# Kernel tuning notes

Hardware: AMD Instinct MI355X
Metric: run time of the kernel (lower is better)

Reference implementation:

```python
import jax, jax.numpy as jnp
import numpy as np

N = 50000      # nodes
E = 800000     # edges (before self loops)
F_DIM = 512    # raw feature dim
HID = 64       # hidden dim (= per-head dim, concat=False)
HEADS = 4
EMB = 64
NEG_SLOPE = 0.2
LN_EPS = 1e-5


def setup_inputs() -> dict:
    key = jax.random.key(0)
    ks = jax.random.split(key, 24)
    rn = lambda k, shape: jax.random.normal(k, shape, dtype=jnp.float32) * 0.05
    inp = {
        'features': jax.random.normal(ks[0], (N, F_DIM), dtype=jnp.float32),
        'edge_index': jax.random.randint(ks[1], (2, E), 0, N),
        'Wt': rn(ks[2], (F_DIM, HID)), 'bt': jnp.zeros((HID,), jnp.float32),
        'Wp': rn(ks[3], (HID, EMB)), 'bp': jnp.zeros((EMB,), jnp.float32),
    }
    for l in range(2):
        o = 4 + l * 4
        inp[f'Wg{l}'] = rn(ks[o], (HID, HEADS * HID))
        inp[f'as{l}'] = rn(ks[o + 1], (HEADS, HID))
        inp[f'ad{l}'] = rn(ks[o + 2], (HEADS, HID))
        inp[f'bg{l}'] = jnp.zeros((HID,), jnp.float32)
        inp[f'g{l}'] = jnp.ones((HID,), jnp.float32)
        inp[f'b{l}'] = jnp.zeros((HID,), jnp.float32)
        inp[f'a{l}'] = jnp.full((1,), 0.25, jnp.float32)  # PReLU weight
    return inp


def gat_block(x, src, dst, Wg, a_src, a_dst, bg, gamma, beta, prelu_a):
    # GATConv (heads=HEADS, concat=False, add_self_loops already in src/dst)
    h = (x @ Wg).reshape(N, HEADS, HID)                    # [N,H,C]
    al_s = jnp.einsum('nhc,hc->nh', h, a_src)              # [N,H]
    al_d = jnp.einsum('nhc,hc->nh', h, a_dst)
    e = jax.nn.leaky_relu(al_s[src] + al_d[dst], NEG_SLOPE)  # [E,H]
    m = jax.ops.segment_max(e, dst, num_segments=N)
    ex = jnp.exp(e - m[dst])
    denom = jax.ops.segment_sum(ex, dst, num_segments=N)
    alpha = ex / denom[dst]                                # segment softmax over in-edges
    out = jax.ops.segment_sum(h[src] * alpha[:, :, None], dst, num_segments=N)  # [N,H,C]
    out = out.mean(axis=1) + bg                            # concat=False -> mean heads
    # LayerNorm
    mu = out.mean(-1, keepdims=True)
    var = ((out - mu) ** 2).mean(-1, keepdims=True)
    xn = (out - mu) / jnp.sqrt(var + LN_EPS) * gamma + beta
    # PReLU
    return jnp.where(xn > 0, xn, prelu_a * xn)


def reference(features, edge_index, Wt, bt, Wp, bp,
              Wg0, as0, ad0, bg0, g0, b0, a0,
              Wg1, as1, ad1, bg1, g1, b1, a1):
    loops = jnp.arange(N)
    src = jnp.concatenate([edge_index[0], loops])
    dst = jnp.concatenate([edge_index[1], loops])
    x = features @ Wt + bt
    x = x + gat_block(x, src, dst, Wg0, as0, ad0, bg0, g0, b0, a0)
    x = x + gat_block(x, src, dst, Wg1, as1, ad1, bg1, g1, b1, a1)
    z = x @ Wp + bp
    return z / jnp.maximum(jnp.linalg.norm(z, axis=-1, keepdims=True), 1e-12)
```

## Files before the change

kernel.cpp:

```cpp
#include <hip/hip_runtime.h>
#include <hip/hip_bf16.h>

typedef __attribute__((ext_vector_type(8))) short bvec8;
typedef __attribute__((ext_vector_type(4))) float fvec4;

__device__ __forceinline__ void splitf(float f, short& hi, short& lo) {
  __hip_bfloat16 h = __float2bfloat16(f);
  float r = f - __bfloat162float(h);
  __hip_bfloat16 l = __float2bfloat16(r);
  hi = *(short*)&h;
  lo = *(short*)&l;
}
__device__ __forceinline__ float bits2f(unsigned short u) {
  unsigned int v = ((unsigned int)u) << 16;
  return __uint_as_float(v);
}

__global__ void k_degree(const int* __restrict__ ei, int* __restrict__ cnt, int E, int N) {
  int i = blockIdx.x * 256 + threadIdx.x;
  if (i >= E + N) return;
  int d = (i < E) ? ei[E + i] : (i - E);
  atomicAdd(&cnt[d], 1);
}

__global__ void k_scan(const int* __restrict__ cnt, int* __restrict__ off, int* __restrict__ cur, int N) {
  __shared__ int wsum[16];
  __shared__ int s_carry;
  int t = threadIdx.x, lane = t & 63, wv = t >> 6;
  if (t == 0) s_carry = 0;
  __syncthreads();
  for (int base = 0; base < N; base += 4096) {
    int idx = base + t * 4;
    int4 v = make_int4(0, 0, 0, 0);
    if (idx < N) v = *(const int4*)(cnt + idx);
    int s0 = v.x, s1 = s0 + v.y, s2 = s1 + v.z, s3 = s2 + v.w;
    int sc = s3;
    #pragma unroll
    for (int d = 1; d < 64; d <<= 1) {
      int u = __shfl_up(sc, d, 64);
      if (lane >= d) sc += u;
    }
    if (lane == 63) wsum[wv] = sc;
    __syncthreads();
    int carry = s_carry;
    int woff = 0;
    #pragma unroll
    for (int w = 0; w < 16; ++w) woff += (w < wv) ? wsum[w] : 0;
    int eb = carry + woff + sc - s3;
    if (idx < N) {
      int4 o = make_int4(eb, eb + s0, eb + s1, eb + s2);
      *(int4*)(off + idx) = o;
      *(int4*)(cur + idx) = o;
    }
    __syncthreads();
    if (t == 1023) s_carry = carry + woff + sc;
    __syncthreads();
  }
  if (t == 0) off[N] = s_carry;
}

__global__ void k_scatter(const int* __restrict__ ei, int* __restrict__ cur, int* __restrict__ csr, int E, int N) {
  int i = blockIdx.x * 256 + threadIdx.x;
  if (i >= E + N) return;
  int s, d;
  if (i < E) { s = ei[i]; d = ei[E + i]; } else { s = i - E; d = i - E; }
  int p = atomicAdd(&cur[d], 1);
  csr[p] = s;
}

__global__ __launch_bounds__(64) void k_wprep(const float* __restrict__ Wg, short* __restrict__ pk) {
  int tile = blockIdx.x;
  int lane = threadIdx.x;
  int w = tile >> 3, s = (tile >> 2) & 1, ct = tile & 3;
  int fq = lane >> 4, fr = lane & 15;
  bvec8 hv, lv;
  #pragma unroll
  for (int j = 0; j < 8; ++j) {
    short hh, ll;
    splitf(Wg[(size_t)(s * 32 + fq * 8 + j) * 256 + w * 64 + ct * 16 + fr], hh, ll);
    hv[j] = hh; lv[j] = ll;
  }
  *(bvec8*)(pk + tile * 1024 + lane * 8) = hv;
  *(bvec8*)(pk + tile * 1024 + 512 + lane * 8) = lv;
}

#define LROW 56
__global__ __launch_bounds__(256) void k_x0(const float* __restrict__ feat, const float* __restrict__ Wt,
                                            const float* __restrict__ bt, float* __restrict__ x, int N) {
  __shared__ __align__(16) short sAh[64 * LROW];
  __shared__ __align__(16) short sAl[64 * LROW];
  __shared__ __align__(16) short sBh[64 * LROW];
  __shared__ __align__(16) short sBl[64 * LROW];

  const int t = threadIdx.x;
  const int lane = t & 63;
  const int w = t >> 6;
  const int fr = lane & 15;
  const int fq = lane >> 4;
  const int n0 = blockIdx.x * 64;

  const int ar = t >> 2;
  const int ac8 = (t & 3) * 8;
  int arow = n0 + ar; if (arow >= N) arow = N - 1;
  const float* fbase = feat + (size_t)arow * 512;
  const int bn = t & 63;
  const int bc8 = (t >> 6) * 8;

  fvec4 acc[4];
  #pragma unroll
  for (int i = 0; i < 4; ++i) acc[i] = (fvec4){0.f, 0.f, 0.f, 0.f};

  for (int s = 0; s < 16; ++s) {
    const int k0 = s * 32;
    __syncthreads();
    {
      float4 f0 = *(const float4*)(fbase + k0 + ac8);
      float4 f1 = *(const float4*)(fbase + k0 + ac8 + 4);
      float fv[8] = {f0.x, f0.y, f0.z, f0.w, f1.x, f1.y, f1.z, f1.w};
      bvec8 hv, lv;
      #pragma unroll
      for (int j = 0; j < 8; ++j) { short h, l; splitf(fv[j], h, l); hv[j] = h; lv[j] = l; }
      *(bvec8*)(sAh + ar * LROW + ac8) = hv;
      *(bvec8*)(sAl + ar * LROW + ac8) = lv;
    }
    {
      bvec8 hv, lv;
      #pragma unroll
      for (int j = 0; j < 8; ++j) {
        float v = Wt[(size_t)(k0 + bc8 + j) * 64 + bn];
        short h, l; splitf(v, h, l); hv[j] = h; lv[j] = l;
      }
      *(bvec8*)(sBh + bn * LROW + bc8) = hv;
      *(bvec8*)(sBl + bn * LROW + bc8) = lv;
    }
    __syncthreads();
    const bvec8 ah = *(const bvec8*)(sAh + (w * 16 + fr) * LROW + fq * 8);
    const bvec8 al = *(const bvec8*)(sAl + (w * 16 + fr) * LROW + fq * 8);
    #pragma unroll
    for (int nt = 0; nt < 4; ++nt) {
      const bvec8 bh = *(const bvec8*)(sBh + (nt * 16 + fr) * LROW + fq * 8);
      const bvec8 bl = *(const bvec8*)(sBl + (nt * 16 + fr) * LROW + fq * 8);
      acc[nt] = __builtin_amdgcn_mfma_f32_16x16x32_bf16(ah, bh, acc[nt], 0, 0, 0);
      acc[nt] = __builtin_amdgcn_mfma_f32_16x16x32_bf16(ah, bl, acc[nt], 0, 0, 0);
      acc[nt] = __builtin_amdgcn_mfma_f32_16x16x32_bf16(al, bh, acc[nt], 0, 0, 0);
    }
  }
  #pragma unroll
  for (int nt = 0; nt < 4; ++nt) {
    float btv = bt[nt * 16 + fr];
    #pragma unroll
    for (int r = 0; r < 4; ++r) {
      int node = n0 + w * 16 + fq * 4 + r;
      if (node < N) x[(size_t)node * 64 + nt * 16 + fr] = acc[nt][r] + btv;
    }
  }
}

#define HROW 72
__global__ __launch_bounds__(256) void k_h(const float* __restrict__ x, const short* __restrict__ pk,
                                           const float* __restrict__ as_, const float* __restrict__ ad_,
                                           __hip_bfloat16* __restrict__ h, float* __restrict__ als,
                                           float* __restrict__ ald, int N) {
  __shared__ __align__(16) short sAh[64 * HROW];
  __shared__ __align__(16) short sAl[64 * HROW];
  const int t = threadIdx.x;
  const int lane = t & 63;
  const int w = t >> 6;
  const int fr = lane & 15;
  const int fq = lane >> 4;
  const int n0 = blockIdx.x * 64;

  {
    int ar = t >> 2;
    int c0 = (t & 3) * 16;
    int arow = n0 + ar; if (arow >= N) arow = N - 1;
    const float* xb = x + (size_t)arow * 64 + c0;
    #pragma unroll
    for (int half = 0; half < 2; ++half) {
      float4 f0 = *(const float4*)(xb + half * 8);
      float4 f1 = *(const float4*)(xb + half * 8 + 4);
      float fv[8] = {f0.x, f0.y, f0.z, f0.w, f1.x, f1.y, f1.z, f1.w};
      bvec8 hv, lv;
      #pragma unroll
      for (int j = 0; j < 8; ++j) { short hh, ll; splitf(fv[j], hh, ll); hv[j] = hh; lv[j] = ll; }
      *(bvec8*)(sAh + ar * HROW + c0 + half * 8) = hv;
      *(bvec8*)(sAl + ar * HROW + c0 + half * 8) = lv;
    }
  }
  bvec8 bh[2][4], bl[2][4];
  #pragma unroll
  for (int s = 0; s < 2; ++s)
    #pragma unroll
    for (int ct = 0; ct < 4; ++ct) {
      int tile = (w * 2 + s) * 4 + ct;
      bh[s][ct] = *(const bvec8*)(pk + tile * 1024 + lane * 8);
      bl[s][ct] = *(const bvec8*)(pk + tile * 1024 + 512 + lane * 8);
    }
  __syncthreads();
  fvec4 acc[4][4];
  #pragma unroll
  for (int nt = 0; nt < 4; ++nt)
    #pragma unroll
    for (int ct = 0; ct < 4; ++ct) acc[nt][ct] = (fvec4){0.f, 0.f, 0.f, 0.f};
  #pragma unroll
  for (int s = 0; s < 2; ++s)
    #pragma unroll
    for (int nt = 0; nt < 4; ++nt) {
      const bvec8 ah = *(const bvec8*)(sAh + (nt * 16 + fr) * HROW + s * 32 + fq * 8);
      const bvec8 al = *(const bvec8*)(sAl + (nt * 16 + fr) * HROW + s * 32 + fq * 8);
      #pragma unroll
      for (int ct = 0; ct < 4; ++ct) {
        acc[nt][ct] = __builtin_amdgcn_mfma_f32_16x16x32_bf16(ah, bh[s][ct], acc[nt][ct], 0, 0, 0);
        acc[nt][ct] = __builtin_amdgcn_mfma_f32_16x16x32_bf16(ah, bl[s][ct], acc[nt][ct], 0, 0, 0);
        acc[nt][ct] = __builtin_amdgcn_mfma_f32_16x16x32_bf16(al, bh[s][ct], acc[nt][ct], 0, 0, 0);
      }
    }
  float asv[4], adv[4];
  #pragma unroll
  for (int ct = 0; ct < 4; ++ct) {
    asv[ct] = as_[w * 64 + ct * 16 + fr];
    adv[ct] = ad_[w * 64 + ct * 16 + fr];
  }
  #pragma unroll
  for (int nt = 0; nt < 4; ++nt) {
    #pragma unroll
    for (int r = 0; r < 4; ++r) {
      int n = n0 + nt * 16 + fq * 4 + r;
      float ps = 0.f, pd = 0.f;
      #pragma unroll
      for (int ct = 0; ct < 4; ++ct) {
        ps = fmaf(acc[nt][ct][r], asv[ct], ps);
        pd = fmaf(acc[nt][ct][r], adv[ct], pd);
      }
      #pragma unroll
      for (int m = 1; m < 16; m <<= 1) { ps += __shfl_xor(ps, m, 64); pd += __shfl_xor(pd, m, 64); }
      if (fr == 0 && n < N) { als[(size_t)n * 4 + w] = ps; ald[(size_t)n * 4 + w] = pd; }
      #pragma unroll
      for (int ct = 0; ct < 4; ++ct)
        if (n < N) h[(size_t)n * 256 + w * 64 + ct * 16 + fr] = __float2bfloat16(acc[nt][ct][r]);
    }
  }
}

template <bool FINAL>
__global__ __launch_bounds__(256) void k_agg(const __hip_bfloat16* __restrict__ h, const float* __restrict__ als,
                                             const float* __restrict__ ald, const int* __restrict__ off,
                                             const int* __restrict__ csr, const float* __restrict__ bg,
                                             const float* __restrict__ gam, const float* __restrict__ bet,
                                             const float* __restrict__ pa, float* __restrict__ x,
                                             const float* __restrict__ Wp, const float* __restrict__ bp,
                                             float* __restrict__ out, int N) {
  int lane = threadIdx.x & 63;
  int n = blockIdx.x * 4 + (threadIdx.x >> 6);
  if (n >= N) return;
  int hh = lane >> 4;
  int cg = (lane & 15) * 4;
  float aldv = ald[(size_t)n * 4 + hh];
  int e0 = __builtin_amdgcn_readfirstlane(off[n]);
  int e1 = __builtin_amdgcn_readfirstlane(off[n + 1]);
  float a0 = 0, a1 = 0, a2 = 0, a3 = 0, den = 0;
  const unsigned short* hb = (const unsigned short*)h;
  const int co = hh * 64 + cg;
  int e = e0;
  for (; e + 4 <= e1; e += 4) {
    int s0 = csr[e + 0], s1 = csr[e + 1], s2 = csr[e + 2], s3 = csr[e + 3];
    float q0 = als[(size_t)s0 * 4 + hh];
    float q1 = als[(size_t)s1 * 4 + hh];
    float q2 = als[(size_t)s2 * 4 + hh];
    float q3 = als[(size_t)s3 * 4 + hh];
    ushort4 g0 = *(const ushort4*)(hb + (size_t)s0 * 256 + co);
    ushort4 g1 = *(const ushort4*)(hb + (size_t)s1 * 256 + co);
    ushort4 g2 = *(const ushort4*)(hb + (size_t)s2 * 256 + co);
    ushort4 g3 = *(const ushort4*)(hb + (size_t)s3 * 256 + co);
    float t0 = q0 + aldv; t0 = fmaxf(t0, 0.2f * t0); float w0 = __expf(t0);
    float t1 = q1 + aldv; t1 = fmaxf(t1, 0.2f * t1); float w1 = __expf(t1);
    float t2 = q2 + aldv; t2 = fmaxf(t2, 0.2f * t2); float w2 = __expf(t2);
    float t3 = q3 + aldv; t3 = fmaxf(t3, 0.2f * t3); float w3 = __expf(t3);
    den += (w0 + w1) + (w2 + w3);
    a0 += w0 * bits2f(g0.x) + w1 * bits2f(g1.x) + w2 * bits2f(g2.x) + w3 * bits2f(g3.x);
    a1 += w0 * bits2f(g0.y) + w1 * bits2f(g1.y) + w2 * bits2f(g2.y) + w3 * bits2f(g3.y);
    a2 += w0 * bits2f(g0.z) + w1 * bits2f(g1.z) + w2 * bits2f(g2.z) + w3 * bits2f(g3.z);
    a3 += w0 * bits2f(g0.w) + w1 * bits2f(g1.w) + w2 * bits2f(g2.w) + w3 * bits2f(g3.w);
  }
  for (; e < e1; ++e) {
    int s = csr[e];
    float t = als[(size_t)s * 4 + hh] + aldv;
    t = fmaxf(t, 0.2f * t);
    float w = __expf(t);
    den += w;
    const ushort4 hv = *(const ushort4*)(hb + (size_t)s * 256 + co);
    a0 += w * bits2f(hv.x); a1 += w * bits2f(hv.y); a2 += w * bits2f(hv.z); a3 += w * bits2f(hv.w);
  }
  float inv = 1.0f / den;
  a0 *= inv; a1 *= inv; a2 *= inv; a3 *= inv;
  a0 += __shfl_xor(a0, 16, 64); a0 += __shfl_xor(a0, 32, 64);
  a1 += __shfl_xor(a1, 16, 64); a1 += __shfl_xor(a1, 32, 64);
  a2 += __shfl_xor(a2, 16, 64); a2 += __shfl_xor(a2, 32, 64);
  a3 += __shfl_xor(a3, 16, 64); a3 += __shfl_xor(a3, 32, 64);
  float v0 = a0 * 0.25f + bg[cg + 0];
  float v1 = a1 * 0.25f + bg[cg + 1];
  float v2 = a2 * 0.25f + bg[cg + 2];
  float v3 = a3 * 0.25f + bg[cg + 3];
  float sum = v0 + v1 + v2 + v3;
  #pragma unroll
  for (int m = 1; m < 16; m <<= 1) sum += __shfl_xor(sum, m, 64);
  float mu = sum * (1.f / 64.f);
  float d0 = v0 - mu, d1 = v1 - mu, d2 = v2 - mu, d3 = v3 - mu;
  float vv = d0 * d0 + d1 * d1 + d2 * d2 + d3 * d3;
  #pragma unroll
  for (int m = 1; m < 16; m <<= 1) vv += __shfl_xor(vv, m, 64);
  float rstd = rsqrtf(vv * (1.f / 64.f) + 1e-5f);
  float A = pa[0];
  float y0 = d0 * rstd * gam[cg + 0] + bet[cg + 0];
  float y1 = d1 * rstd * gam[cg + 1] + bet[cg + 1];
  float y2 = d2 * rstd * gam[cg + 2] + bet[cg + 2];
  float y3 = d3 * rstd * gam[cg + 3] + bet[cg + 3];
  y0 = y0 > 0.f ? y0 : A * y0;
  y1 = y1 > 0.f ? y1 : A * y1;
  y2 = y2 > 0.f ? y2 : A * y2;
  y3 = y3 > 0.f ? y3 : A * y3;
  float o0 = 0.f, o1 = 0.f, o2 = 0.f, o3 = 0.f;
  if (lane < 16) {
    float4 xo = *(const float4*)(x + (size_t)n * 64 + cg);
    o0 = xo.x + y0; o1 = xo.y + y1; o2 = xo.z + y2; o3 = xo.w + y3;
  }
  if (!FINAL) {
    if (lane < 16) {
      float4 o = make_float4(o0, o1, o2, o3);
      *(float4*)(x + (size_t)n * 64 + cg) = o;
    }
  } else {
    float acc = bp[lane];
    #pragma unroll
    for (int g = 0; g < 16; ++g) {
      float rx = __shfl(o0, g, 64), ry = __shfl(o1, g, 64);
      float rz = __shfl(o2, g, 64), rw = __shfl(o3, g, 64);
      const float* wp = Wp + g * 4 * 64 + lane;
      acc = fmaf(rx, wp[0],   acc);
      acc = fmaf(ry, wp[64],  acc);
      acc = fmaf(rz, wp[128], acc);
      acc = fmaf(rw, wp[192], acc);
    }
    float sq = acc * acc;
    #pragma unroll
    for (int m = 1; m < 64; m <<= 1) sq += __shfl_xor(sq, m, 64);
    float nrm = fmaxf(sqrtf(sq), 1e-12f);
    out[(size_t)n * 64 + lane] = acc / nrm;
  }
}

extern "C" void kernel_launch(void* const* d_in, const int* in_sizes, int n_in,
                              void* d_out, int out_size, void* d_ws, size_t ws_size,
                              hipStream_t stream) {
  const float* feat = (const float*)d_in[0];
  const int*   ei   = (const int*)d_in[1];
  const float* Wt   = (const float*)d_in[2];
  const float* bt   = (const float*)d_in[3];
  const float* Wp   = (const float*)d_in[4];
  const float* bp   = (const float*)d_in[5];
  const float* Wg[2]  = {(const float*)d_in[6],  (const float*)d_in[13]};
  const float* as_[2] = {(const float*)d_in[7],  (const float*)d_in[14]};
  const float* ad_[2] = {(const float*)d_in[8],  (const float*)d_in[15]};
  const float* bg[2]  = {(const float*)d_in[9],  (const float*)d_in[16]};
  const float* gm[2]  = {(const float*)d_in[10], (const float*)d_in[17]};
  const float* be[2]  = {(const float*)d_in[11], (const float*)d_in[18]};
  const float* pa[2]  = {(const float*)d_in[12], (const float*)d_in[19]};

  const int N = in_sizes[0] / 512;
  const int E = in_sizes[1] / 2;

  float* x = (float*)d_ws;
  __hip_bfloat16* hb = (__hip_bfloat16*)(x + (size_t)N * 64);
  float* als = (float*)((short*)hb + (size_t)N * 256);
  float* ald = als + (size_t)N * 4;
  int* cnt = (int*)(ald + (size_t)N * 4);
  int* cur = cnt + N;
  int* csr = cur + N;
  int* off = csr + (E + N);
  short* pk0 = (short*)(((uintptr_t)(off + N + 1) + 15) & ~(uintptr_t)15);
  short* pk1 = pk0 + 32768;

  hipMemsetAsync(cnt, 0, (size_t)N * sizeof(int), stream);
  int eb = (E + N + 255) / 256;
  k_degree<<<eb, 256, 0, stream>>>(ei, cnt, E, N);
  k_scan<<<1, 1024, 0, stream>>>(cnt, off, cur, N);
  k_scatter<<<eb, 256, 0, stream>>>(ei, cur, csr, E, N);
  k_wprep<<<32, 64, 0, stream>>>(Wg[0], pk0);
  k_wprep<<<32, 64, 0, stream>>>(Wg[1], pk1);

  int nb4 = (N + 3) / 4;
  int nb64 = (N + 63) / 64;
  k_x0<<<nb64, 256, 0, stream>>>(feat, Wt, bt, x, N);

  k_h<<<nb64, 256, 0, stream>>>(x, pk0, as_[0], ad_[0], hb, als, ald, N);
  k_agg<false><<<nb4, 256, 0, stream>>>(hb, als, ald, off, csr, bg[0], gm[0], be[0], pa[0], x,
                                        Wp, bp, (float*)d_out, N);
  k_h<<<nb64, 256, 0, stream>>>(x, pk1, as_[1], ad_[1], hb, als, ald, N);
  k_agg<true><<<nb4, 256, 0, stream>>>(hb, als, ald, off, csr, bg[1], gm[1], be[1], pa[1], x,
                                       Wp, bp, (float*)d_out, N);
}
```

Measured before the change: 489.0 us.

## Store x as pre-split bf16 hi/lo, prepack Wt, parallelize CSR scan

The node state x is now kept as two bf16 planes (hi and lo), so k_h feeds MFMA operands straight from global memory without an LDS staging pass and a per-use split. Wt is prepacked into MFMA fragment layout in a merged prep kernel, and k_x0 now handles 128 rows per block with no shared memory or barriers. The single-block sequential scan is replaced by a three-kernel block scan, top-level scan and add. This trades extra kernel launches and a slightly different rounding of x (hi+lo, roughly 16 mantissa bits) for fewer syncs and less LDS traffic.

Result: no change. 485.6 us (-0.7%).

```diff
diff --git a/kernel.cpp b/kernel.cpp
--- a/kernel.cpp
+++ b/kernel.cpp
@@ -23,40 +23,51 @@
   atomicAdd(&cnt[d], 1);
 }
 
-__global__ void k_scan(const int* __restrict__ cnt, int* __restrict__ off, int* __restrict__ cur, int N) {
+__global__ __launch_bounds__(1024) void k_scan_blk(const int* __restrict__ cnt, int* __restrict__ off,
+                                                   int* __restrict__ bsum, int N) {
   __shared__ int wsum[16];
-  __shared__ int s_carry;
   int t = threadIdx.x, lane = t & 63, wv = t >> 6;
-  if (t == 0) s_carry = 0;
+  int idx = blockIdx.x * 4096 + t * 4;
+  int4 v = make_int4(0, 0, 0, 0);
+  if (idx < N) v = *(const int4*)(cnt + idx);
+  int s0 = v.x, s1 = s0 + v.y, s2 = s1 + v.z, s3 = s2 + v.w;
+  int sc = s3;
+  #pragma unroll
+  for (int d = 1; d < 64; d <<= 1) {
+    int u = __shfl_up(sc, d, 64);
+    if (lane >= d) sc += u;
+  }
+  if (lane == 63) wsum[wv] = sc;
   __syncthreads();
-  for (int base = 0; base < N; base += 4096) {
-    int idx = base + t * 4;
-    int4 v = make_int4(0, 0, 0, 0);
-    if (idx < N) v = *(const int4*)(cnt + idx);
-    int s0 = v.x, s1 = s0 + v.y, s2 = s1 + v.z, s3 = s2 + v.w;
-    int sc = s3;
-    #pragma unroll
-    for (int d = 1; d < 64; d <<= 1) {
-      int u = __shfl_up(sc, d, 64);
-      if (lane >= d) sc += u;
-    }
-    if (lane == 63) wsum[wv] = sc;
-    __syncthreads();
-    int carry = s_carry;
-    int woff = 0;
-    #pragma unroll
-    for (int w = 0; w < 16; ++w) woff += (w < wv) ? wsum[w] : 0;
-    int eb = carry + woff + sc - s3;
-    if (idx < N) {
-      int4 o = make_int4(eb, eb + s0, eb + s1, eb + s2);
-      *(int4*)(off + idx) = o;
-      *(int4*)(cur + idx) = o;
-    }
-    __syncthreads();
-    if (t == 1023) s_carry = carry + woff + sc;
-    __syncthreads();
-  }
-  if (t == 0) off[N] = s_carry;
+  int woff = 0;
+  #pragma unroll
+  for (int w = 0; w < 16; ++w) woff += (w < wv) ? wsum[w] : 0;
+  int eb = woff + sc - s3;
+  if (idx < N) {
+    int4 o = make_int4(eb, eb + s0, eb + s1, eb + s2);
+    *(int4*)(off + idx) = o;
+  }
+  if (t == 1023) bsum[blockIdx.x] = woff + sc;
+}
+
+__global__ void k_scan_top(int* __restrict__ bsum, int* __restrict__ off, int nb, int N) {
+  if (threadIdx.x == 0) {
+    int ex = 0;
+    for (int i = 0; i < nb; ++i) { int tv = bsum[i]; bsum[i] = ex; ex += tv; }
+    off[N] = ex;
+  }
+}
+
+__global__ __launch_bounds__(1024) void k_scan_add(int* __restrict__ off, int* __restrict__ cur,
+                                                   const int* __restrict__ bsum, int N) {
+  int t = threadIdx.x;
+  int idx = blockIdx.x * 4096 + t * 4;
+  if (idx >= N) return;
+  int b = bsum[blockIdx.x];
+  int4 o = *(const int4*)(off + idx);
+  o.x += b; o.y += b; o.z += b; o.w += b;
+  *(int4*)(off + idx) = o;
+  *(int4*)(cur + idx) = o;
 }
 
 __global__ void k_scatter(const int* __restrict__ ei, int* __restrict__ cur, int* __restrict__ csr, int E, int N) {
@@ -68,30 +79,109 @@
   csr[p] = s;
 }
 
-__global__ __launch_bounds__(64) void k_wprep(const float* __restrict__ Wg, short* __restrict__ pk) {
-  int tile = blockIdx.x;
+__global__ __launch_bounds__(64) void k_prep(const float* __restrict__ Wg0, const float* __restrict__ Wg1,
+                                             const float* __restrict__ Wt,
+                                             short* __restrict__ pk0, short* __restrict__ pk1,
+                                             short* __restrict__ wtpk) {
+  int b = blockIdx.x;
   int lane = threadIdx.x;
-  int w = tile >> 3, s = (tile >> 2) & 1, ct = tile & 3;
   int fq = lane >> 4, fr = lane & 15;
   bvec8 hv, lv;
-  #pragma unroll
-  for (int j = 0; j < 8; ++j) {
-    short hh, ll;
-    splitf(Wg[(size_t)(s * 32 + fq * 8 + j) * 256 + w * 64 + ct * 16 + fr], hh, ll);
-    hv[j] = hh; lv[j] = ll;
-  }
-  *(bvec8*)(pk + tile * 1024 + lane * 8) = hv;
-  *(bvec8*)(pk + tile * 1024 + 512 + lane * 8) = lv;
-}
-
-#define LROW 56
-__global__ __launch_bounds__(256) void k_x0(const float* __restrict__ feat, const float* __restrict__ Wt,
-                                            const float* __restrict__ bt, float* __restrict__ x, int N) {
-  __shared__ __align__(16) short sAh[64 * LROW];
-  __shared__ __align__(16) short sAl[64 * LROW];
-  __shared__ __align__(16) short sBh[64 * LROW];
-  __shared__ __align__(16) short sBl[64 * LROW];
-
+  if (b < 64) {
+    const float* Wg = (b < 32) ? Wg0 : Wg1;
+    short* pk = (b < 32) ? pk0 : pk1;
+    int tile = b & 31;
+    int w = tile >> 3, s = (tile >> 2) & 1, ct = tile & 3;
+    #pragma unroll
+    for (int j = 0; j < 8; ++j) {
+      short hh, ll;
+      splitf(Wg[(size_t)(s * 32 + fq * 8 + j) * 256 + w * 64 + ct * 16 + fr], hh, ll);
+      hv[j] = hh; lv[j] = ll;
+    }
+    *(bvec8*)(pk + tile * 1024 + lane * 8) = hv;
+    *(bvec8*)(pk + tile * 1024 + 512 + lane * 8) = lv;
+  } else {
+    int tile = b - 64;
+    int s = tile >> 2, nt = tile & 3;
+    #pragma unroll
+    for (int j = 0; j < 8; ++j) {
+      short hh, ll;
+      splitf(Wt[(size_t)(s * 32 + fq * 8 + j) * 64 + nt * 16 + fr], hh, ll);
+      hv[j] = hh; lv[j] = ll;
+    }
+    *(bvec8*)(wtpk + tile * 1024 + lane * 8) = hv;
+    *(bvec8*)(wtpk + tile * 1024 + 512 + lane * 8) = lv;
+  }
+}
+
+__global__ __launch_bounds__(256) void k_x0(const float* __restrict__ feat, const short* __restrict__ wtpk,
+                                            const float* __restrict__ bt,
+                                            short* __restrict__ xhi, short* __restrict__ xlo, int N) {
+  const int t = threadIdx.x;
+  const int lane = t & 63;
+  const int w = t >> 6;
+  const int fr = lane & 15;
+  const int fq = lane >> 4;
+  const int n0 = blockIdx.x * 128;
+
+  int ar0 = n0 + w * 32 + fr;      if (ar0 >= N) ar0 = N - 1;
+  int ar1 = n0 + w * 32 + 16 + fr; if (ar1 >= N) ar1 = N - 1;
+  const float* fb0 = feat + (size_t)ar0 * 512 + fq * 8;
+  const float* fb1 = feat + (size_t)ar1 * 512 + fq * 8;
+
+  fvec4 acc[2][4];
+  #pragma unroll
+  for (int m = 0; m < 2; ++m)
+    #pragma unroll
+    for (int nt = 0; nt < 4; ++nt) acc[m][nt] = (fvec4){0.f, 0.f, 0.f, 0.f};
+
+  for (int s = 0; s < 16; ++s) {
+    bvec8 bh[4], bl[4];
+    #pragma unroll
+    for (int nt = 0; nt < 4; ++nt) {
+      bh[nt] = *(const bvec8*)(wtpk + (s * 4 + nt) * 1024 + lane * 8);
+      bl[nt] = *(const bvec8*)(wtpk + (s * 4 + nt) * 1024 + 512 + lane * 8);
+    }
+    #pragma unroll
+    for (int m = 0; m < 2; ++m) {
+      const float* fb = m ? fb1 : fb0;
+      float4 f0 = *(const float4*)(fb + s * 32);
+      float4 f1 = *(const float4*)(fb + s * 32 + 4);
+      float fv[8] = {f0.x, f0.y, f0.z, f0.w, f1.x, f1.y, f1.z, f1.w};
+      bvec8 ah, al;
+      #pragma unroll
+      for (int j = 0; j < 8; ++j) { short hh, ll; splitf(fv[j], hh, ll); ah[j] = hh; al[j] = ll; }
+      #pragma unroll
+      for (int nt = 0; nt < 4; ++nt) {
+        acc[m][nt] = __builtin_amdgcn_mfma_f32_16x16x32_bf16(ah, bh[nt], acc[m][nt], 0, 0, 0);
+        acc[m][nt] = __builtin_amdgcn_mfma_f32_16x16x32_bf16(ah, bl[nt], acc[m][nt], 0, 0, 0);
+        acc[m][nt] = __builtin_amdgcn_mfma_f32_16x16x32_bf16(al, bh[nt], acc[m][nt], 0, 0, 0);
+      }
+    }
+  }
+  #pragma unroll
+  for (int m = 0; m < 2; ++m)
+    #pragma unroll
+    for (int nt = 0; nt < 4; ++nt) {
+      float btv = bt[nt * 16 + fr];
+      #pragma unroll
+      for (int r = 0; r < 4; ++r) {
+        int node = n0 + w * 32 + m * 16 + fq * 4 + r;
+        if (node < N) {
+          short hh, ll;
+          splitf(acc[m][nt][r] + btv, hh, ll);
+          xhi[(size_t)node * 64 + nt * 16 + fr] = hh;
+          xlo[(size_t)node * 64 + nt * 16 + fr] = ll;
+        }
+      }
+    }
+}
+
+__global__ __launch_bounds__(256) void k_h(const short* __restrict__ xhi, const short* __restrict__ xlo,
+                                           const short* __restrict__ pk,
+                                           const float* __restrict__ as_, const float* __restrict__ ad_,
+                                           __hip_bfloat16* __restrict__ h, float* __restrict__ als,
+                                           float* __restrict__ ald, int N) {
   const int t = threadIdx.x;
   const int lane = t & 63;
   const int w = t >> 6;
@@ -99,94 +189,6 @@
   const int fq = lane >> 4;
   const int n0 = blockIdx.x * 64;
 
-  const int ar = t >> 2;
-  const int ac8 = (t & 3) * 8;
-  int arow = n0 + ar; if (arow >= N) arow = N - 1;
-  const float* fbase = feat + (size_t)arow * 512;
-  const int bn = t & 63;
-  const int bc8 = (t >> 6) * 8;
-
-  fvec4 acc[4];
-  #pragma unroll
-  for (int i = 0; i < 4; ++i) acc[i] = (fvec4){0.f, 0.f, 0.f, 0.f};
-
-  for (int s = 0; s < 16; ++s) {
-    const int k0 = s * 32;
-    __syncthreads();
-    {
-      float4 f0 = *(const float4*)(fbase + k0 + ac8);
-      float4 f1 = *(const float4*)(fbase + k0 + ac8 + 4);
-      float fv[8] = {f0.x, f0.y, f0.z, f0.w, f1.x, f1.y, f1.z, f1.w};
-      bvec8 hv, lv;
-      #pragma unroll
-      for (int j = 0; j < 8; ++j) { short h, l; splitf(fv[j], h, l); hv[j] = h; lv[j] = l; }
-      *(bvec8*)(sAh + ar * LROW + ac8) = hv;
-      *(bvec8*)(sAl + ar * LROW + ac8) = lv;
-    }
-    {
-      bvec8 hv, lv;
-      #pragma unroll
-      for (int j = 0; j < 8; ++j) {
-        float v = Wt[(size_t)(k0 + bc8 + j) * 64 + bn];
-        short h, l; splitf(v, h, l); hv[j] = h; lv[j] = l;
-      }
-      *(bvec8*)(sBh + bn * LROW + bc8) = hv;
-      *(bvec8*)(sBl + bn * LROW + bc8) = lv;
-    }
-    __syncthreads();
-    const bvec8 ah = *(const bvec8*)(sAh + (w * 16 + fr) * LROW + fq * 8);
-    const bvec8 al = *(const bvec8*)(sAl + (w * 16 + fr) * LROW + fq * 8);
-    #pragma unroll
-    for (int nt = 0; nt < 4; ++nt) {
-      const bvec8 bh = *(const bvec8*)(sBh + (nt * 16 + fr) * LROW + fq * 8);
-      const bvec8 bl = *(const bvec8*)(sBl + (nt * 16 + fr) * LROW + fq * 8);
-      acc[nt] = __builtin_amdgcn_mfma_f32_16x16x32_bf16(ah, bh, acc[nt], 0, 0, 0);
-      acc[nt] = __builtin_amdgcn_mfma_f32_16x16x32_bf16(ah, bl, acc[nt], 0, 0, 0);
-      acc[nt] = __builtin_amdgcn_mfma_f32_16x16x32_bf16(al, bh, acc[nt], 0, 0, 0);
-    }
-  }
-  #pragma unroll
-  for (int nt = 0; nt < 4; ++nt) {
-    float btv = bt[nt * 16 + fr];
-    #pragma unroll
-    for (int r = 0; r < 4; ++r) {
-      int node = n0 + w * 16 + fq * 4 + r;
-      if (node < N) x[(size_t)node * 64 + nt * 16 + fr] = acc[nt][r] + btv;
-    }
-  }
-}
-
-#define HROW 72
-__global__ __launch_bounds__(256) void k_h(const float* __restrict__ x, const short* __restrict__ pk,
-                                           const float* __restrict__ as_, const float* __restrict__ ad_,
-                                           __hip_bfloat16* __restrict__ h, float* __restrict__ als,
-                                           float* __restrict__ ald, int N) {
-  __shared__ __align__(16) short sAh[64 * HROW];
-  __shared__ __align__(16) short sAl[64 * HROW];
-  const int t = threadIdx.x;
-  const int lane = t & 63;
-  const int w = t >> 6;
-  const int fr = lane & 15;
-  const int fq = lane >> 4;
-  const int n0 = blockIdx.x * 64;
-
-  {
-    int ar = t >> 2;
-    int c0 = (t & 3) * 16;
-    int arow = n0 + ar; if (arow >= N) arow = N - 1;
-    const float* xb = x + (size_t)arow * 64 + c0;
-    #pragma unroll
-    for (int half = 0; half < 2; ++half) {
-      float4 f0 = *(const float4*)(xb + half * 8);
-      float4 f1 = *(const float4*)(xb + half * 8 + 4);
-      float fv[8] = {f0.x, f0.y, f0.z, f0.w, f1.x, f1.y, f1.z, f1.w};
-      bvec8 hv, lv;
-      #pragma unroll
-      for (int j = 0; j < 8; ++j) { short hh, ll; splitf(fv[j], hh, ll); hv[j] = hh; lv[j] = ll; }
-      *(bvec8*)(sAh + ar * HROW + c0 + half * 8) = hv;
-      *(bvec8*)(sAl + ar * HROW + c0 + half * 8) = lv;
-    }
-  }
   bvec8 bh[2][4], bl[2][4];
   #pragma unroll
   for (int s = 0; s < 2; ++s)
@@ -196,18 +198,20 @@
       bh[s][ct] = *(const bvec8*)(pk + tile * 1024 + lane * 8);
       bl[s][ct] = *(const bvec8*)(pk + tile * 1024 + 512 + lane * 8);
     }
-  __syncthreads();
   fvec4 acc[4][4];
   #pragma unroll
   for (int nt = 0; nt < 4; ++nt)
     #pragma unroll
     for (int ct = 0; ct < 4; ++ct) acc[nt][ct] = (fvec4){0.f, 0.f, 0.f, 0.f};
   #pragma unroll
-  for (int s = 0; s < 2; ++s)
-    #pragma unroll
-    for (int nt = 0; nt < 4; ++nt) {
-      const bvec8 ah = *(const bvec8*)(sAh + (nt * 16 + fr) * HROW + s * 32 + fq * 8);
-      const bvec8 al = *(const bvec8*)(sAl + (nt * 16 + fr) * HROW + s * 32 + fq * 8);
+  for (int nt = 0; nt < 4; ++nt) {
+    int row = n0 + nt * 16 + fr; if (row >= N) row = N - 1;
+    const short* xh = xhi + (size_t)row * 64 + fq * 8;
+    const short* xl = xlo + (size_t)row * 64 + fq * 8;
+    #pragma unroll
+    for (int s = 0; s < 2; ++s) {
+      const bvec8 ah = *(const bvec8*)(xh + s * 32);
+      const bvec8 al = *(const bvec8*)(xl + s * 32);
       #pragma unroll
       for (int ct = 0; ct < 4; ++ct) {
         acc[nt][ct] = __builtin_amdgcn_mfma_f32_16x16x32_bf16(ah, bh[s][ct], acc[nt][ct], 0, 0, 0);
@@ -215,6 +219,7 @@
         acc[nt][ct] = __builtin_amdgcn_mfma_f32_16x16x32_bf16(al, bh[s][ct], acc[nt][ct], 0, 0, 0);
       }
     }
+  }
   float asv[4], adv[4];
   #pragma unroll
   for (int ct = 0; ct < 4; ++ct) {
@@ -247,7 +252,8 @@
                                              const float* __restrict__ ald, const int* __restrict__ off,
                                              const int* __restrict__ csr, const float* __restrict__ bg,
                                              const float* __restrict__ gam, const float* __restrict__ bet,
-                                             const float* __restrict__ pa, float* __restrict__ x,
+                                             const float* __restrict__ pa,
+                                             short* __restrict__ xhi, short* __restrict__ xlo,
                                              const float* __restrict__ Wp, const float* __restrict__ bp,
                                              float* __restrict__ out, int N) {
   int lane = threadIdx.x & 63;
@@ -321,13 +327,21 @@
   y3 = y3 > 0.f ? y3 : A * y3;
   float o0 = 0.f, o1 = 0.f, o2 = 0.f, o3 = 0.f;
   if (lane < 16) {
-    float4 xo = *(const float4*)(x + (size_t)n * 64 + cg);
-    o0 = xo.x + y0; o1 = xo.y + y1; o2 = xo.z + y2; o3 = xo.w + y3;
+    ushort4 xh = *(const ushort4*)((const unsigned short*)xhi + (size_t)n * 64 + cg);
+    ushort4 xl = *(const ushort4*)((const unsigned short*)xlo + (size_t)n * 64 + cg);
+    o0 = bits2f(xh.x) + bits2f(xl.x) + y0;
+    o1 = bits2f(xh.y) + bits2f(xl.y) + y1;
+    o2 = bits2f(xh.z) + bits2f(xl.z) + y2;
+    o3 = bits2f(xh.w) + bits2f(xl.w) + y3;
   }
   if (!FINAL) {
     if (lane < 16) {
-      float4 o = make_float4(o0, o1, o2, o3);
-      *(float4*)(x + (size_t)n * 64 + cg) = o;
+      short h0, l0, h1, l1, h2, l2, h3, l3;
+      splitf(o0, h0, l0); splitf(o1, h1, l1); splitf(o2, h2, l2); splitf(o3, h3, l3);
+      ushort4 oh = make_ushort4((unsigned short)h0, (unsigned short)h1, (unsigned short)h2, (unsigned short)h3);
+      ushort4 ol = make_ushort4((unsigned short)l0, (unsigned short)l1, (unsigned short)l2, (unsigned short)l3);
+      *(ushort4*)((unsigned short*)xhi + (size_t)n * 64 + cg) = oh;
+      *(ushort4*)((unsigned short*)xlo + (size_t)n * 64 + cg) = ol;
     }
   } else {
     float acc = bp[lane];
@@ -369,33 +383,39 @@
   const int N = in_sizes[0] / 512;
   const int E = in_sizes[1] / 2;
 
-  float* x = (float*)d_ws;
-  __hip_bfloat16* hb = (__hip_bfloat16*)(x + (size_t)N * 64);
+  short* xhi = (short*)d_ws;
+  short* xlo = xhi + (size_t)N * 64;
+  __hip_bfloat16* hb = (__hip_bfloat16*)(xlo + (size_t)N * 64);
   float* als = (float*)((short*)hb + (size_t)N * 256);
   float* ald = als + (size_t)N * 4;
   int* cnt = (int*)(ald + (size_t)N * 4);
   int* cur = cnt + N;
   int* csr = cur + N;
   int* off = csr + (E + N);
-  short* pk0 = (short*)(((uintptr_t)(off + N + 1) + 15) & ~(uintptr_t)15);
+  int* bsum = off + (N + 1);
+  short* pk0 = (short*)(((uintptr_t)(bsum + 16) + 15) & ~(uintptr_t)15);
   short* pk1 = pk0 + 32768;
+  short* wtpk = pk1 + 32768;
 
   hipMemsetAsync(cnt, 0, (size_t)N * sizeof(int), stream);
   int eb = (E + N + 255) / 256;
+  int SB = (N + 4095) / 4096;
   k_degree<<<eb, 256, 0, stream>>>(ei, cnt, E, N);
-  k_scan<<<1, 1024, 0, stream>>>(cnt, off, cur, N);
+  k_prep<<<128, 64, 0, stream>>>(Wg[0], Wg[1], Wt, pk0, pk1, wtpk);
+  k_scan_blk<<<SB, 1024, 0, stream>>>(cnt, off, bsum, N);
+  k_scan_top<<<1, 64, 0, stream>>>(bsum, off, SB, N);
+  k_scan_add<<<SB, 1024, 0, stream>>>(off, cur, bsum, N);
   k_scatter<<<eb, 256, 0, stream>>>(ei, cur, csr, E, N);
-  k_wprep<<<32, 64, 0, stream>>>(Wg[0], pk0);
-  k_wprep<<<32, 64, 0, stream>>>(Wg[1], pk1);
 
   int nb4 = (N + 3) / 4;
   int nb64 = (N + 63) / 64;
-  k_x0<<<nb64, 256, 0, stream>>>(feat, Wt, bt, x, N);
-
-  k_h<<<nb64, 256, 0, stream>>>(x, pk0, as_[0], ad_[0], hb, als, ald, N);
-  k_agg<false><<<nb4, 256, 0, stream>>>(hb, als, ald, off, csr, bg[0], gm[0], be[0], pa[0], x,
-                                        Wp, bp, (float*)d_out, N);
-  k_h<<<nb64, 256, 0, stream>>>(x, pk1, as_[1], ad_[1], hb, als, ald, N);
-  k_agg<true><<<nb4, 256, 0, stream>>>(hb, als, ald, off, csr, bg[1], gm[1], be[1], pa[1], x,
-                                       Wp, bp, (float*)d_out, N);
-}
+  int nb128 = (N + 127) / 128;
+  k_x0<<<nb128, 256, 0, stream>>>(feat, wtpk, bt, xhi, xlo, N);
+
+  k_h<<<nb64, 256, 0, stream>>>(xhi, xlo, pk0, as_[0], ad_[0], hb, als, ald, N);
+  k_agg<false><<<nb4, 256, 0, stream>>>(hb, als, ald, off, csr, bg[0], gm[0], be[0], pa[0],
+                                        xhi, xlo, Wp, bp, (float*)d_out, N);
+  k_h<<<nb64, 256, 0, stream>>>(xhi, xlo, pk1, as_[1], ad_[1], hb, als, ald, N);
+  k_agg<true><<<nb4, 256, 0, stream>>>(hb, als, ald, off, csr, bg[1], gm[1], be[1], pa[1],
+                                       xhi, xlo, Wp, bp, (float*)d_out, N);
+}
```
